# Performance work log

Measured on AMD Instinct MI355X. Metric: run time of the kernel, lower is better.

Reference implementation:

```python
import jax, jax.numpy as jnp
import numpy as np

L = 2048      # seq_len
E = 2048      # hidden_dim
H = 16        # num_heads
D = E // H    # head_dim


def setup_inputs() -> dict:
    key = jax.random.key(0)
    ks = jax.random.split(key, 6)
    x = jax.random.normal(ks[0], (L, E), dtype=jnp.float32)
    bias_matrix = jax.random.normal(ks[1], (L, L), dtype=jnp.float32) * 0.1
    # nn.MultiheadAttention params: packed in_proj [3E, E] + bias [3E], out_proj [E, E] + bias [E]
    in_proj_weight = jax.random.normal(ks[2], (3 * E, E), dtype=jnp.float32) * 0.02
    in_proj_bias = jax.random.normal(ks[3], (3 * E,), dtype=jnp.float32) * 0.02
    out_proj_weight = jax.random.normal(ks[4], (E, E), dtype=jnp.float32) * 0.02
    out_proj_bias = jax.random.normal(ks[5], (E,), dtype=jnp.float32) * 0.02
    return {
        "x": x,
        "bias_matrix": bias_matrix,
        "in_proj_weight": in_proj_weight,
        "in_proj_bias": in_proj_bias,
        "out_proj_weight": out_proj_weight,
        "out_proj_bias": out_proj_bias,
    }


def reference(x, bias_matrix, in_proj_weight, in_proj_bias, out_proj_weight, out_proj_bias):
    # Packed QKV projection (torch Linear convention: y = x @ W.T + b)
    qkv = x @ in_proj_weight.T + in_proj_bias            # [L, 3E]
    q, k, v = jnp.split(qkv, 3, axis=-1)                 # each [L, E]
    q = q.reshape(L, H, D)
    k = k.reshape(L, H, D)
    v = v.reshape(L, H, D)
    scale = 1.0 / jnp.sqrt(jnp.asarray(D, dtype=x.dtype))
    # scores: [H, L, L]; bias_matrix broadcast over heads (torch 2D attn_mask semantics)
    scores = jnp.einsum("lhd,mhd->hlm", q * scale, k) + bias_matrix[None, :, :]
    attn = jax.nn.softmax(scores, axis=-1)
    ctx = jnp.einsum("hlm,mhd->lhd", attn, v).reshape(L, E)
    out = ctx @ out_proj_weight.T + out_proj_bias        # [L, E]
    return out
```

## Files before the change

### kernel.cpp

```cpp
#include <hip/hip_runtime.h>
#include <math.h>

#define L_SEQ 2048
#define E_DIM 2048
#define H_NUM 16
#define D_HEAD 128

typedef __attribute__((ext_vector_type(8))) _Float16 half8;
typedef __attribute__((ext_vector_type(4))) _Float16 half4;
typedef __attribute__((ext_vector_type(4))) float floatx4;

static __device__ __forceinline__ void gload16(const void* g, void* lds) {
  __builtin_amdgcn_global_load_lds(
      (const __attribute__((address_space(1))) void*)g,
      (__attribute__((address_space(3))) void*)lds, 16, 0, 0);
}

__global__ __launch_bounds__(256)
void cvt3_f32_f16(const float* __restrict__ a, _Float16* __restrict__ oa, int na,
                  const float* __restrict__ b, _Float16* __restrict__ ob, int nb,
                  const float* __restrict__ c, _Float16* __restrict__ oc, int nc) {
  int i = (blockIdx.x * 256 + threadIdx.x) * 8;
  const float* src;
  _Float16* dst;
  if (i < na) {
    src = a + i; dst = oa + i;
  } else if (i < na + nb) {
    src = b + (i - na); dst = ob + (i - na);
  } else if (i < na + nb + nc) {
    src = c + (i - na - nb); dst = oc + (i - na - nb);
  } else {
    return;
  }
  float4 p = *(const float4*)src;
  float4 q = *(const float4*)(src + 4);
  half8 h = {(_Float16)p.x, (_Float16)p.y, (_Float16)p.z, (_Float16)p.w,
             (_Float16)q.x, (_Float16)q.y, (_Float16)q.z, (_Float16)q.w};
  *(half8*)dst = h;
}

__global__ __launch_bounds__(512, 1)
void gemm_qkv(const _Float16* __restrict__ A, const _Float16* __restrict__ B,
              const float* __restrict__ bias, _Float16* __restrict__ qk,
              _Float16* __restrict__ vt) {
  constexpr int K = E_DIM;
  __shared__ __align__(16) char smem[131072];
  char* const Asm = smem;
  char* const Bsm = smem + 65536;

  const int tid = threadIdx.x;
  const int wave = tid >> 6, lane = tid & 63;
  const int l15 = lane & 15, quad = lane >> 4;
  const int wm = wave >> 2, wn = wave & 3;
  const int brow = blockIdx.y * 256, bcol = blockIdx.x * 256;

  const _Float16* Ag = A + (size_t)brow * K;
  const _Float16* Bg = B + (size_t)bcol * K;

  auto stg = [&](char* smbase, const _Float16* gbase, int T, int kh) {
    char* slot = smbase + ((T & 1) * 2 + kh) * 16384;
#pragma unroll
    for (int j = 0; j < 2; ++j) {
      int mb = j * 512 + (tid & ~63);
      int m = mb + (tid & 63);
      int row = m >> 2, c = m & 3;
      gload16(gbase + (size_t)row * K + T * 64 + kh * 32 + ((c ^ (row & 3)) * 8),
              slot + mb * 16);
    }
  };

  floatx4 acc[8][4];
#pragma unroll
  for (int i = 0; i < 8; ++i)
#pragma unroll
    for (int j = 0; j < 4; ++j) acc[i][j] = (floatx4){0.f, 0.f, 0.f, 0.f};

  auto compute_phase = [&](int T, int ks) {
    const char* Ab = Asm + ((T & 1) * 2 + ks) * 16384;
    const char* Bb = Bsm + ((T & 1) * 2 + ks) * 16384;
    half8 af[8], bf[4];
#pragma unroll
    for (int t = 0; t < 8; ++t)
      af[t] = *(const half8*)(Ab + (size_t)(wm * 128 + t * 16 + l15) * 64 +
                              ((quad ^ (l15 & 3)) * 16));
#pragma unroll
    for (int t = 0; t < 4; ++t)
      bf[t] = *(const half8*)(Bb + (size_t)(wn * 64 + t * 16 + l15) * 64 +
                              ((quad ^ (l15 & 3)) * 16));
#pragma unroll
    for (int i = 0; i < 8; ++i)
#pragma unroll
      for (int j = 0; j < 4; ++j)
        acc[i][j] = __builtin_amdgcn_mfma_f32_16x16x32_f16(af[i], bf[j],
                                                           acc[i][j], 0, 0, 0);
  };

  stg(Asm, Ag, 0, 0); stg(Bsm, Bg, 0, 0);
  stg(Asm, Ag, 0, 1); stg(Bsm, Bg, 0, 1);
  stg(Asm, Ag, 1, 0); stg(Bsm, Bg, 1, 0);

  for (int T = 0; T < 31; ++T) {
    __builtin_amdgcn_sched_barrier(0);
    asm volatile("s_waitcnt vmcnt(8) lgkmcnt(0)" ::: "memory");
    __builtin_amdgcn_s_barrier();
    __builtin_amdgcn_sched_barrier(0);
    stg(Asm, Ag, T + 1, 1);
    stg(Bsm, Bg, T + 1, 1);
    compute_phase(T, 0);
    __builtin_amdgcn_sched_barrier(0);
    asm volatile("s_waitcnt vmcnt(8) lgkmcnt(0)" ::: "memory");
    __builtin_amdgcn_s_barrier();
    __builtin_amdgcn_sched_barrier(0);
    if (T < 30) {
      stg(Asm, Ag, T + 2, 0);
      stg(Bsm, Bg, T + 2, 0);
    }
    compute_phase(T, 1);
  }
  __builtin_amdgcn_sched_barrier(0);
  asm volatile("s_waitcnt vmcnt(4) lgkmcnt(0)" ::: "memory");
  __builtin_amdgcn_s_barrier();
  __builtin_amdgcn_sched_barrier(0);
  compute_phase(31, 0);
  __builtin_amdgcn_sched_barrier(0);
  asm volatile("s_waitcnt vmcnt(0) lgkmcnt(0)" ::: "memory");
  __builtin_amdgcn_s_barrier();
  __builtin_amdgcn_sched_barrier(0);
  compute_phase(31, 1);

  const int crow = brow + wm * 128;
  const int ccol0 = bcol + wn * 64;
  if (bcol < 2 * E_DIM) {
#pragma unroll
    for (int j = 0; j < 4; ++j) {
      int col = ccol0 + j * 16 + l15;
      float bb = bias[col];
#pragma unroll
      for (int i = 0; i < 8; ++i)
#pragma unroll
        for (int r = 0; r < 4; ++r)
          qk[(size_t)(crow + i * 16 + quad * 4 + r) * (2 * E_DIM) + col] =
              (_Float16)(acc[i][j][r] + bb);
    }
  } else {
#pragma unroll
    for (int j = 0; j < 4; ++j) {
      int col = ccol0 + j * 16 + l15;
      float bb = bias[col];
      int vrow = col - 2 * E_DIM;
#pragma unroll
      for (int i = 0; i < 8; ++i) {
        int rbase = crow + i * 16 + quad * 4;
        half4 h = {(_Float16)(acc[i][j][0] + bb), (_Float16)(acc[i][j][1] + bb),
                   (_Float16)(acc[i][j][2] + bb), (_Float16)(acc[i][j][3] + bb)};
        *(half4*)&vt[(size_t)vrow * L_SEQ + rbase] = h;
      }
    }
  }
}

template <int TM, int TN, int WR, int WC>
__global__ __launch_bounds__(256)
void gemm_mfma(const _Float16* __restrict__ A, const _Float16* __restrict__ B,
               const float* __restrict__ bias, float* __restrict__ C,
               int M, int N, int K) {
  constexpr int RT = TM / (16 * WR);
  constexpr int CT = TN / (16 * WC);
  constexpr int ACH = TM / 8;
  constexpr int NCH = (TM + TN) / 32;

  __shared__ _Float16 As[2][TM * 64];
  __shared__ _Float16 Bs[2][TN * 64];

  const int tid = threadIdx.x;
  const int wave = tid >> 6, lane = tid & 63;
  const int l15 = lane & 15, quad = lane >> 4;
  const int wr = wave / WC, wc = wave % WC;
  const int row0 = blockIdx.y * TM, col0 = blockIdx.x * TN;

  const int srow = lane >> 3;
  const int gc = (lane & 7) ^ srow;

  auto stage = [&](int buf, int k0) {
#pragma unroll
    for (int c = 0; c < NCH; ++c) {
      int chunk = wave * NCH + c;
      if (chunk < ACH) {
        int row = chunk * 8 + srow;
        gload16((const char*)(A + (size_t)(row0 + row) * K + k0) + gc * 16,
                (char*)&As[buf][0] + chunk * 1024);
      } else {
        int bch = chunk - ACH;
        int row = bch * 8 + srow;
        gload16((const char*)(B + (size_t)(col0 + row) * K + k0) + gc * 16,
                (char*)&Bs[buf][0] + bch * 1024);
      }
    }
  };

  floatx4 acc[RT][CT];
#pragma unroll
  for (int i = 0; i < RT; ++i)
#pragma unroll
    for (int j = 0; j < CT; ++j) acc[i][j] = (floatx4){0.f, 0.f, 0.f, 0.f};

  const int niter = K / 64;
  stage(0, 0);

  for (int it = 0; it < niter; ++it) {
    const int cur = it & 1;
    __syncthreads();
    if (it + 1 < niter) stage(cur ^ 1, (it + 1) * 64);

#pragma unroll
    for (int ks = 0; ks < 2; ++ks) {
      half8 af[RT], bf[CT];
#pragma unroll
      for (int t = 0; t < RT; ++t) {
        int r = wr * (16 * RT) + t * 16 + l15;
        af[t] = *(const half8*)&As[cur][r * 64 + (((ks * 4 + quad) ^ (r & 7)) * 8)];
      }
#pragma unroll
      for (int t = 0; t < CT; ++t) {
        int r = wc * (16 * CT) + t * 16 + l15;
        bf[t] = *(const half8*)&Bs[cur][r * 64 + (((ks * 4 + quad) ^ (r & 7)) * 8)];
      }
#pragma unroll
      for (int tr = 0; tr < RT; ++tr)
#pragma unroll
        for (int tc = 0; tc < CT; ++tc)
          acc[tr][tc] = __builtin_amdgcn_mfma_f32_16x16x32_f16(
              af[tr], bf[tc], acc[tr][tc], 0, 0, 0);
    }
  }

  const int crow = row0 + wr * (16 * RT);
  const int ccol = col0 + wc * (16 * CT);

#pragma unroll
  for (int tc = 0; tc < CT; ++tc) {
    int col = ccol + tc * 16 + l15;
    float bb = bias[col];
#pragma unroll
    for (int tr = 0; tr < RT; ++tr)
#pragma unroll
      for (int r = 0; r < 4; ++r)
        C[(size_t)(crow + tr * 16 + quad * 4 + r) * N + col] =
            acc[tr][tc][r] + bb;
  }
}

__global__ __launch_bounds__(512, 2)
void attn_mfma(const _Float16* __restrict__ qk, const _Float16* __restrict__ vt,
               const float* __restrict__ bias, _Float16* __restrict__ ctx) {
  const int h = blockIdx.x;
  const int q0 = blockIdx.y * 128;
  const int tid = threadIdx.x;
  const int wave = tid >> 6;
  const int lane = tid & 63;
  const int l15 = lane & 15;
  const int quad = lane >> 4;

  __shared__ _Float16 Ks[2][64][136];
  __shared__ _Float16 Vst[2][128][72];
  __shared__ _Float16 Ps[128][72];

  half8 qa[4];
  {
    const _Float16* qp = qk + (size_t)(q0 + wave * 16 + l15) * (2 * E_DIM) +
                         h * D_HEAD + quad * 8;
#pragma unroll
    for (int ks = 0; ks < 4; ++ks) qa[ks] = *(const half8*)(qp + ks * 32);
  }

  float l_i = 0.f;
  floatx4 o[8];
#pragma unroll
  for (int t = 0; t < 8; ++t) o[t] = (floatx4){0.f, 0.f, 0.f, 0.f};

  const float scale = 0.088388347648318447f;

  half8 kreg[2], vreg[2];
  floatx4 bcur[4], bnxt[4];
#pragma unroll
  for (int c = 0; c < 2; ++c) {
    int m = c * 512 + tid;
    kreg[c] = *(const half8*)(qk + (size_t)(m >> 4) * (2 * E_DIM) + E_DIM +
                              h * D_HEAD + (m & 15) * 8);
    vreg[c] = *(const half8*)(vt + (size_t)(h * D_HEAD + (m >> 3)) * L_SEQ +
                              (m & 7) * 8);
  }
#pragma unroll
  for (int t = 0; t < 4; ++t)
    bcur[t] = *(const floatx4*)&bias[(size_t)(q0 + wave * 16 + l15) * L_SEQ +
                                    16 * t + quad * 4];
#pragma unroll
  for (int c = 0; c < 2; ++c) {
    int m = c * 512 + tid;
    *(half8*)&Ks[0][m >> 4][(m & 15) * 8] = kreg[c];
    *(half8*)&Vst[0][m >> 3][(m & 7) * 8] = vreg[c];
  }

#pragma unroll 2
  for (int it = 0; it < 32; ++it) {
    const int cur = it & 1, nxt = cur ^ 1;
    const int kt = it * 64;
    __syncthreads();

    if (it < 31) {
#pragma unroll
      for (int c = 0; c < 2; ++c) {
        int m = c * 512 + tid;
        kreg[c] = *(const half8*)(qk + (size_t)(kt + 64 + (m >> 4)) * (2 * E_DIM) +
                                  E_DIM + h * D_HEAD + (m & 15) * 8);
        vreg[c] = *(const half8*)(vt + (size_t)(h * D_HEAD + (m >> 3)) * L_SEQ +
                                  kt + 64 + (m & 7) * 8);
      }
#pragma unroll
      for (int t = 0; t < 4; ++t)
        bnxt[t] = *(const floatx4*)&bias[(size_t)(q0 + wave * 16 + l15) * L_SEQ +
                                         kt + 64 + 16 * t + quad * 4];
    }

    floatx4 st[4];
#pragma unroll
    for (int t = 0; t < 4; ++t) st[t] = (floatx4){0.f, 0.f, 0.f, 0.f};
#pragma unroll
    for (int ks = 0; ks < 4; ++ks)
#pragma unroll
      for (int t = 0; t < 4; ++t) {
        half8 kf = *(const half8*)&Ks[cur][16 * t + l15][ks * 32 + quad * 8];
        st[t] = __builtin_amdgcn_mfma_f32_16x16x32_f16(kf, qa[ks], st[t], 0, 0, 0);
      }

    {
      float ls = 0.f;
      float ps[4][4];
#pragma unroll
      for (int t = 0; t < 4; ++t)
#pragma unroll
        for (int r = 0; r < 4; ++r) {
          float p = __expf(fmaf(st[t][r], scale, bcur[t][r]));
          ps[t][r] = p;
          ls += p;
        }
      ls += __shfl_xor(ls, 16);
      ls += __shfl_xor(ls, 32);
      l_i += ls;
#pragma unroll
      for (int t = 0; t < 4; ++t) {
        half4 hp = {(_Float16)ps[t][0], (_Float16)ps[t][1],
                    (_Float16)ps[t][2], (_Float16)ps[t][3]};
        *(half4*)&Ps[wave * 16 + l15][16 * t + quad * 4] = hp;
      }
    }

    half8 pa[2];
#pragma unroll
    for (int ks = 0; ks < 2; ++ks)
      pa[ks] = *(const half8*)&Ps[wave * 16 + l15][ks * 32 + quad * 8];
#pragma unroll
    for (int t = 0; t < 8; ++t)
#pragma unroll
      for (int ks = 0; ks < 2; ++ks) {
        half8 vf = *(const half8*)&Vst[cur][16 * t + l15][ks * 32 + quad * 8];
        o[t] = __builtin_amdgcn_mfma_f32_16x16x32_f16(pa[ks], vf, o[t], 0, 0, 0);
      }

    if (it < 31) {
#pragma unroll
      for (int c = 0; c < 2; ++c) {
        int m = c * 512 + tid;
        *(half8*)&Ks[nxt][m >> 4][(m & 15) * 8] = kreg[c];
        *(half8*)&Vst[nxt][m >> 3][(m & 7) * 8] = vreg[c];
      }
#pragma unroll
      for (int t = 0; t < 4; ++t) bcur[t] = bnxt[t];
    }
  }

  float inv[4];
#pragma unroll
  for (int r = 0; r < 4; ++r) inv[r] = 1.f / __shfl(l_i, quad * 4 + r);
#pragma unroll
  for (int t = 0; t < 8; ++t)
#pragma unroll
    for (int r = 0; r < 4; ++r) {
      int row = q0 + wave * 16 + quad * 4 + r;
      ctx[(size_t)row * E_DIM + h * D_HEAD + 16 * t + l15] =
          (_Float16)(o[t][r] * inv[r]);
    }
}

extern "C" void kernel_launch(void* const* d_in, const int* in_sizes, int n_in,
                              void* d_out, int out_size, void* d_ws, size_t ws_size,
                              hipStream_t stream) {
  const float* x          = (const float*)d_in[0];
  const float* bias_mat   = (const float*)d_in[1];
  const float* in_proj_w  = (const float*)d_in[2];
  const float* in_proj_b  = (const float*)d_in[3];
  const float* out_proj_w = (const float*)d_in[4];
  const float* out_proj_b = (const float*)d_in[5];
  float* out = (float*)d_out;

  _Float16* x16 = (_Float16*)d_ws;
  _Float16* w1  = x16 + (size_t)L_SEQ * E_DIM;
  _Float16* w2  = w1 + (size_t)3 * E_DIM * E_DIM;
  _Float16* qk  = w2 + (size_t)E_DIM * E_DIM;
  _Float16* vt  = qk + (size_t)L_SEQ * 2 * E_DIM;
  _Float16* ctx = vt + (size_t)E_DIM * L_SEQ;

  dim3 blk(256);
  const int nx = L_SEQ * E_DIM, nw1 = 3 * E_DIM * E_DIM, nw2 = E_DIM * E_DIM;

  cvt3_f32_f16<<<(nx + nw1 + nw2) / 2048, blk, 0, stream>>>(
      x, x16, nx, in_proj_w, w1, nw1, out_proj_w, w2, nw2);

  gemm_qkv<<<dim3(3 * E_DIM / 256, L_SEQ / 256), dim3(512), 0, stream>>>(
      x16, w1, in_proj_b, qk, vt);

  attn_mfma<<<dim3(H_NUM, L_SEQ / 128), dim3(512), 0, stream>>>(qk, vt, bias_mat,
                                                                ctx);

  gemm_mfma<128, 64, 4, 1><<<dim3(E_DIM / 64, L_SEQ / 128), blk, 0, stream>>>(
      ctx, w2, out_proj_b, out, L_SEQ, E_DIM, E_DIM);
}
```

Measured before the change: 281.2 us.

## Retile QKV GEMM to 128x384 blocks with swizzled block order

```diff
diff --git a/kernel.cpp b/kernel.cpp
--- a/kernel.cpp
+++ b/kernel.cpp
@@ -46,75 +46,84 @@
   constexpr int K = E_DIM;
   __shared__ __align__(16) char smem[131072];
   char* const Asm = smem;
-  char* const Bsm = smem + 65536;
+  char* const Bsm = smem + 32768;
 
   const int tid = threadIdx.x;
   const int wave = tid >> 6, lane = tid & 63;
   const int l15 = lane & 15, quad = lane >> 4;
   const int wm = wave >> 2, wn = wave & 3;
-  const int brow = blockIdx.y * 256, bcol = blockIdx.x * 256;
+
+  const int lid = blockIdx.y * 16 + blockIdx.x;
+  const int swz = (lid & 7) * 32 + (lid >> 3);
+  const int brow = (swz >> 4) * 128, bcol = (swz & 15) * 384;
 
   const _Float16* Ag = A + (size_t)brow * K;
   const _Float16* Bg = B + (size_t)bcol * K;
 
-  auto stg = [&](char* smbase, const _Float16* gbase, int T, int kh) {
-    char* slot = smbase + ((T & 1) * 2 + kh) * 16384;
-#pragma unroll
-    for (int j = 0; j < 2; ++j) {
+  auto stg = [&](int T, int kh) {
+    char* aslot = Asm + ((T & 1) * 2 + kh) * 8192;
+    char* bslot = Bsm + ((T & 1) * 2 + kh) * 24576;
+    {
+      int row = tid >> 2, c = tid & 3;
+      gload16(Ag + (size_t)row * K + T * 64 + kh * 32 +
+                  ((c ^ ((row >> 1) & 3)) * 8),
+              aslot + (tid & ~63) * 16);
+    }
+#pragma unroll
+    for (int j = 0; j < 3; ++j) {
       int mb = j * 512 + (tid & ~63);
       int m = mb + (tid & 63);
       int row = m >> 2, c = m & 3;
-      gload16(gbase + (size_t)row * K + T * 64 + kh * 32 + ((c ^ (row & 3)) * 8),
-              slot + mb * 16);
+      gload16(Bg + (size_t)row * K + T * 64 + kh * 32 +
+                  ((c ^ ((row >> 1) & 3)) * 8),
+              bslot + mb * 16);
     }
   };
 
-  floatx4 acc[8][4];
-#pragma unroll
-  for (int i = 0; i < 8; ++i)
-#pragma unroll
-    for (int j = 0; j < 4; ++j) acc[i][j] = (floatx4){0.f, 0.f, 0.f, 0.f};
+  floatx4 acc[4][6];
+#pragma unroll
+  for (int i = 0; i < 4; ++i)
+#pragma unroll
+    for (int j = 0; j < 6; ++j) acc[i][j] = (floatx4){0.f, 0.f, 0.f, 0.f};
 
   auto compute_phase = [&](int T, int ks) {
-    const char* Ab = Asm + ((T & 1) * 2 + ks) * 16384;
-    const char* Bb = Bsm + ((T & 1) * 2 + ks) * 16384;
-    half8 af[8], bf[4];
-#pragma unroll
-    for (int t = 0; t < 8; ++t)
-      af[t] = *(const half8*)(Ab + (size_t)(wm * 128 + t * 16 + l15) * 64 +
-                              ((quad ^ (l15 & 3)) * 16));
-#pragma unroll
-    for (int t = 0; t < 4; ++t)
-      bf[t] = *(const half8*)(Bb + (size_t)(wn * 64 + t * 16 + l15) * 64 +
-                              ((quad ^ (l15 & 3)) * 16));
-#pragma unroll
-    for (int i = 0; i < 8; ++i)
-#pragma unroll
-      for (int j = 0; j < 4; ++j)
+    const char* Ab = Asm + ((T & 1) * 2 + ks) * 8192;
+    const char* Bb = Bsm + ((T & 1) * 2 + ks) * 24576;
+    half8 af[4], bf[6];
+#pragma unroll
+    for (int t = 0; t < 4; ++t) {
+      int r = wm * 64 + t * 16 + l15;
+      af[t] = *(const half8*)(Ab + (size_t)r * 64 +
+                              ((quad ^ ((r >> 1) & 3)) * 16));
+    }
+#pragma unroll
+    for (int t = 0; t < 6; ++t) {
+      int r = wn * 96 + t * 16 + l15;
+      bf[t] = *(const half8*)(Bb + (size_t)r * 64 +
+                              ((quad ^ ((r >> 1) & 3)) * 16));
+    }
+#pragma unroll
+    for (int i = 0; i < 4; ++i)
+#pragma unroll
+      for (int j = 0; j < 6; ++j)
         acc[i][j] = __builtin_amdgcn_mfma_f32_16x16x32_f16(af[i], bf[j],
                                                            acc[i][j], 0, 0, 0);
   };
 
-  stg(Asm, Ag, 0, 0); stg(Bsm, Bg, 0, 0);
-  stg(Asm, Ag, 0, 1); stg(Bsm, Bg, 0, 1);
-  stg(Asm, Ag, 1, 0); stg(Bsm, Bg, 1, 0);
+  stg(0, 0); stg(0, 1); stg(1, 0);
 
   for (int T = 0; T < 31; ++T) {
     __builtin_amdgcn_sched_barrier(0);
     asm volatile("s_waitcnt vmcnt(8) lgkmcnt(0)" ::: "memory");
     __builtin_amdgcn_s_barrier();
     __builtin_amdgcn_sched_barrier(0);
-    stg(Asm, Ag, T + 1, 1);
-    stg(Bsm, Bg, T + 1, 1);
+    stg(T + 1, 1);
     compute_phase(T, 0);
     __builtin_amdgcn_sched_barrier(0);
     asm volatile("s_waitcnt vmcnt(8) lgkmcnt(0)" ::: "memory");
     __builtin_amdgcn_s_barrier();
     __builtin_amdgcn_sched_barrier(0);
-    if (T < 30) {
-      stg(Asm, Ag, T + 2, 0);
-      stg(Bsm, Bg, T + 2, 0);
-    }
+    if (T < 30) stg(T + 2, 0);
     compute_phase(T, 1);
   }
   __builtin_amdgcn_sched_barrier(0);
@@ -128,28 +137,23 @@
   __builtin_amdgcn_sched_barrier(0);
   compute_phase(31, 1);
 
-  const int crow = brow + wm * 128;
-  const int ccol0 = bcol + wn * 64;
-  if (bcol < 2 * E_DIM) {
-#pragma unroll
-    for (int j = 0; j < 4; ++j) {
-      int col = ccol0 + j * 16 + l15;
-      float bb = bias[col];
-#pragma unroll
-      for (int i = 0; i < 8; ++i)
+  const int crow = brow + wm * 64;
+  const int ccol0 = bcol + wn * 96;
+#pragma unroll
+  for (int j = 0; j < 6; ++j) {
+    int col = ccol0 + j * 16 + l15;
+    float bb = bias[col];
+    if (col < 2 * E_DIM) {
+#pragma unroll
+      for (int i = 0; i < 4; ++i)
 #pragma unroll
         for (int r = 0; r < 4; ++r)
           qk[(size_t)(crow + i * 16 + quad * 4 + r) * (2 * E_DIM) + col] =
               (_Float16)(acc[i][j][r] + bb);
-    }
-  } else {
-#pragma unroll
-    for (int j = 0; j < 4; ++j) {
-      int col = ccol0 + j * 16 + l15;
-      float bb = bias[col];
+    } else {
       int vrow = col - 2 * E_DIM;
 #pragma unroll
-      for (int i = 0; i < 8; ++i) {
+      for (int i = 0; i < 4; ++i) {
         int rbase = crow + i * 16 + quad * 4;
         half4 h = {(_Float16)(acc[i][j][0] + bb), (_Float16)(acc[i][j][1] + bb),
                    (_Float16)(acc[i][j][2] + bb), (_Float16)(acc[i][j][3] + bb)};
@@ -416,8 +420,7 @@
   cvt3_f32_f16<<<(nx + nw1 + nw2) / 2048, blk, 0, stream>>>(
       x, x16, nx, in_proj_w, w1, nw1, out_proj_w, w2, nw2);
 
-  gemm_qkv<<<dim3(3 * E_DIM / 256, L_SEQ / 256), dim3(512), 0, stream>>>(
-      x16, w1, in_proj_b, qk, vt);
+  gemm_qkv<<<dim3(16, 16), dim3(512), 0, stream>>>(x16, w1, in_proj_b, qk, vt);
 
   attn_mfma<<<dim3(H_NUM, L_SEQ / 128), dim3(512), 0, stream>>>(qk, vt, bias_mat,
                                                                 ctx);
```

Result: faster. 275.2 us (median of 2 runs) (-2.1%).
